# Kernel optimization log

Measured on AMD Instinct MI355X. Metric: run time of the kernel, lower is better.

The kernel has to match this reference:

```python
import jax, jax.numpy as jnp
import numpy as np

N_TYPES = 4
N_DESC = 8
K_MAX = 8
R_C = 5.0
L_MAX = 4
N_ATOMS = 10000
M_NBR = 20


def chebyshev_basis(r, r_c, k_max):
    fc = jnp.where(r < r_c, 0.5 * jnp.cos(jnp.pi * r / r_c) + 0.5, jnp.zeros_like(r))
    x = 2.0 * (r / r_c - 1.0) ** 2 - 1.0
    fn = [jnp.ones_like(x), x]
    for _ in range(2, k_max):
        fn.append(2.0 * x * fn[-1] - fn[-2])
    fn = jnp.stack(fn[:k_max], axis=-1)  # [T, k_max]
    return (fn + 1.0) * (0.5 * fc)[..., None]


def legendre_basis(cos_theta, l_max):
    pl = [jnp.ones_like(cos_theta), cos_theta]
    for l in range(2, l_max):
        pl.append(((2 * l - 1) * cos_theta * pl[-1] - (l - 1) * pl[-2]) / l)
    return jnp.stack(pl[:l_max], axis=-1)  # [T, l_max]


def setup_inputs() -> dict:
    key = jax.random.key(0)
    k1, k2, k3, k4 = jax.random.split(key, 4)
    types = jax.random.randint(k1, (N_ATOMS,), 0, N_TYPES)
    # small box so pair distances mostly fall under the cutoff r_c
    positions = jax.random.uniform(k2, (N_ATOMS, 3), dtype=jnp.float32) * 4.0
    # all neighbor slots valid (no -1 padding) and never the atom itself
    offs = jax.random.randint(k3, (N_ATOMS, M_NBR), 1, N_ATOMS)
    angular_neighbors = (jnp.arange(N_ATOMS)[:, None] + offs) % N_ATOMS
    c_table = jax.random.normal(k4, (N_TYPES, N_TYPES, N_DESC, K_MAX), dtype=jnp.float32)
    return {"types": types, "positions": positions,
            "angular_neighbors": angular_neighbors, "c_table": c_table}


def reference(types, positions, angular_neighbors, c_table):
    N, M = angular_neighbors.shape
    ju, ku = np.triu_indices(M, 1)  # P = M*(M-1)//2 pairs per atom
    P = ju.shape[0]
    j_idx = angular_neighbors[:, ju].reshape(-1)  # [N*P]
    k_idx = angular_neighbors[:, ku].reshape(-1)
    i_idx = jnp.repeat(jnp.arange(N), P)

    pos_i = positions[i_idx]
    rij = positions[j_idx] - pos_i
    rik = positions[k_idx] - pos_i
    r_ij = jnp.linalg.norm(rij, axis=-1)
    r_ik = jnp.linalg.norm(rik, axis=-1)
    cos_theta = jnp.sum(rij * rik, axis=-1) / (r_ij * r_ik + 1e-8)

    type_i = types[i_idx]
    f_ij = chebyshev_basis(r_ij, R_C, K_MAX)  # [T, k]
    f_ik = chebyshev_basis(r_ik, R_C, K_MAX)
    c_ij = c_table[type_i, types[j_idx]]  # [T, n_desc, k]
    c_ik = c_table[type_i, types[k_idx]]
    g_ij = jnp.einsum('tdk,tk->td', c_ij, f_ij)  # [T, n_desc]
    g_ik = jnp.einsum('tdk,tk->td', c_ik, f_ik)

    P_l = legendre_basis(cos_theta, L_MAX)  # [T, l_max]
    ang = (g_ij * g_ik)[:, :, None] * P_l[:, None, :]  # [T, n_desc, l_max]
    q = jax.ops.segment_sum(ang, i_idx, num_segments=N)  # [N, n_desc, l_max]
    return q
```

## Files before the change

kernel.cpp:

```cpp
#include <hip/hip_runtime.h>

#define N_TYPES 4
#define N_DESC  8
#define K_MAX   8
#define L_MAX   4
#define M_NBR   20
#define NCOMP   20
#define ATOMS_PER_BLOCK 4

constexpr float R_C  = 5.0f;
constexpr float SQ2  = 1.41421356237309515f;
constexpr float SQ3  = 1.73205080756887729f;
constexpr float SQ6  = 2.44948974968163702f;

__global__ __launch_bounds__(256) void AngularDescriptor_kernel(
    const int*   __restrict__ types,
    const float* __restrict__ pos,
    const int*   __restrict__ nbr,
    const float* __restrict__ c_table,
    float*       __restrict__ out,
    int N)
{
    __shared__ float sfeat[ATOMS_PER_BLOCK][NCOMP][M_NBR];
    __shared__ float scheb[ATOMS_PER_BLOCK][M_NBR][K_MAX];
    __shared__ float sg   [ATOMS_PER_BLOCK][N_DESC][M_NBR];
    __shared__ int   stj  [ATOMS_PER_BLOCK][M_NBR];

    const int t    = threadIdx.x;
    const int w    = t >> 6;
    const int lane = t & 63;
    const int atom = blockIdx.x * ATOMS_PER_BLOCK + w;

    float px = 0.f, py = 0.f, pz = 0.f;
    int ti = 0;
    if (atom < N) {
        ti = types[atom];
        px = pos[atom * 3 + 0];
        py = pos[atom * 3 + 1];
        pz = pos[atom * 3 + 2];
    }

    if (atom < N && lane < M_NBR) {
        const int j = nbr[atom * M_NBR + lane];
        const float dx = pos[j * 3 + 0] - px;
        const float dy = pos[j * 3 + 1] - py;
        const float dz = pos[j * 3 + 2] - pz;
        const float r2   = dx * dx + dy * dy + dz * dz;
        const float rinv = __builtin_amdgcn_rsqf(r2);
        const float r    = r2 * rinv;

        const float fc  = (r < R_C) ? (0.5f * __builtin_amdgcn_cosf(r * (0.5f / R_C)) + 0.5f)
                                    : 0.0f;
        const float hfc = 0.5f * fc;
        const float u   = r * (1.0f / R_C) - 1.0f;
        const float x   = 2.0f * u * u - 1.0f;
        float ch[K_MAX];
        ch[0] = 2.0f * hfc;
        ch[1] = (x + 1.0f) * hfc;
        float tkm2 = 1.0f, tkm1 = x;
        #pragma unroll
        for (int k = 2; k < K_MAX; ++k) {
            const float tk = 2.0f * x * tkm1 - tkm2;
            ch[k] = (tk + 1.0f) * hfc;
            tkm2 = tkm1; tkm1 = tk;
        }
        ((float4*)&scheb[w][lane][0])[0] = make_float4(ch[0], ch[1], ch[2], ch[3]);
        ((float4*)&scheb[w][lane][0])[1] = make_float4(ch[4], ch[5], ch[6], ch[7]);
        stj[w][lane] = types[j];

        const float ux = dx * rinv, uy = dy * rinv, uz = dz * rinv;
        const float x2 = ux * ux, y2 = uy * uy, z2 = uz * uz;
        float F[NCOMP];
        F[0]  = 1.0f;
        F[1]  = ux;  F[2] = uy;  F[3] = uz;
        F[4]  = x2 - (1.0f / 3.0f);
        F[5]  = y2 - (1.0f / 3.0f);
        F[6]  = z2 - (1.0f / 3.0f);
        F[7]  = SQ2 * ux * uy;
        F[8]  = SQ2 * ux * uz;
        F[9]  = SQ2 * uy * uz;
        F[10] = ux * (x2 - 0.6f);
        F[11] = uy * (y2 - 0.6f);
        F[12] = uz * (z2 - 0.6f);
        F[13] = SQ3 * uy * (x2 - 0.2f);
        F[14] = SQ3 * uz * (x2 - 0.2f);
        F[15] = SQ3 * ux * (y2 - 0.2f);
        F[16] = SQ3 * uz * (y2 - 0.2f);
        F[17] = SQ3 * ux * (z2 - 0.2f);
        F[18] = SQ3 * uy * (z2 - 0.2f);
        F[19] = SQ6 * ux * uy * uz;
        #pragma unroll
        for (int c = 0; c < NCOMP; ++c) sfeat[w][c][lane] = F[c];
    }
    __syncthreads();

    const int d  = lane & 7;
    const int gp = lane >> 3;

    if (atom < N) {
        #pragma unroll
        for (int m = gp; m < M_NBR; m += 8) {
            const int tj = stj[w][m];
            const float* c = c_table + (((ti * N_TYPES + tj) * N_DESC + d) * K_MAX);
            const float4 c0 = ((const float4*)c)[0];
            const float4 c1 = ((const float4*)c)[1];
            const float4 f0 = ((const float4*)&scheb[w][m][0])[0];
            const float4 f1 = ((const float4*)&scheb[w][m][0])[1];
            sg[w][d][m] = c0.x * f0.x + c0.y * f0.y + c0.z * f0.z + c0.w * f0.w
                        + c1.x * f1.x + c1.y * f1.y + c1.z * f1.z + c1.w * f1.w;
        }
    }
    __syncthreads();

    float p0 = 0.f, p1 = 0.f, p2 = 0.f, p3 = 0.f;
    float hG2 = 0.f;
    if (atom < N) {
        float g[M_NBR];
        #pragma unroll
        for (int i = 0; i < 5; ++i) {
            const float4 v = ((const float4*)&sg[w][d][0])[i];
            g[4*i+0] = v.x; g[4*i+1] = v.y; g[4*i+2] = v.z; g[4*i+3] = v.w;
        }
        float G2 = 0.f;
        #pragma unroll
        for (int m = 0; m < M_NBR; ++m) G2 = fmaf(g[m], g[m], G2);
        hG2 = 0.5f * G2;

        #pragma unroll
        for (int s = 0; s < 3; ++s) {
            const int c = gp + 8 * s;
            if (c < NCOMP) {
                float acc = 0.f;
                #pragma unroll
                for (int i = 0; i < 5; ++i) {
                    const float4 v = ((const float4*)&sfeat[w][c][0])[i];
                    acc = fmaf(g[4*i+0], v.x, acc);
                    acc = fmaf(g[4*i+1], v.y, acc);
                    acc = fmaf(g[4*i+2], v.z, acc);
                    acc = fmaf(g[4*i+3], v.w, acc);
                }
                const float v2 = acc * acc;
                if      (c == 0)  p0 += 0.50f * v2;
                else if (c <= 3)  p1 += 0.50f * v2;
                else if (c <= 9)  p2 += 0.75f * v2;
                else              p3 += 1.25f * v2;
            }
        }
    }

    #pragma unroll
    for (int off = 8; off <= 32; off <<= 1) {
        p0 += __shfl_xor(p0, off, 64);
        p1 += __shfl_xor(p1, off, 64);
        p2 += __shfl_xor(p2, off, 64);
        p3 += __shfl_xor(p3, off, 64);
    }

    if (atom < N && lane < 8) {
        ((float4*)out)[atom * N_DESC + d] =
            make_float4(p0 - hG2, p1 - hG2, p2 - hG2, p3 - hG2);
    }
}

extern "C" void kernel_launch(void* const* d_in, const int* in_sizes, int n_in,
                              void* d_out, int out_size, void* d_ws, size_t ws_size,
                              hipStream_t stream) {
    const int*   types   = (const int*)  d_in[0];
    const float* pos     = (const float*)d_in[1];
    const int*   nbr     = (const int*)  d_in[2];
    const float* c_table = (const float*)d_in[3];
    float*       out     = (float*)      d_out;

    const int N = in_sizes[0];
    const int grid = (N + ATOMS_PER_BLOCK - 1) / ATOMS_PER_BLOCK;
    AngularDescriptor_kernel<<<grid, 256, 0, stream>>>(types, pos, nbr, c_table, out, N);
}
```

Measured before the change: 66.08 us.

## Pack 16 atoms per block with flat neighbor work distribution and per-thread accumulation

Replaces the one-wavefront-per-atom mapping, where 44 of 64 lanes sat idle in the neighbor phase, with a flat loop over 16 atoms x 20 neighbors spread across all 256 threads. Each neighbor thread now computes its 8 descriptor projections directly from the Chebyshev basis, which removes one barrier phase and the scheb/stj shared buffers. The final phase gives each (atom, desc) pair to one thread that accumulates all 20 angular components in registers, replacing the shuffle reduction. Shared-memory writes are rotated to reduce bank conflicts. In exchange, only 128 of 256 threads are active in the last phase and register pressure rises.

```diff
diff --git a/kernel.cpp b/kernel.cpp
--- a/kernel.cpp
+++ b/kernel.cpp
@@ -3,17 +3,18 @@
 #define N_TYPES 4
 #define N_DESC  8
 #define K_MAX   8
-#define L_MAX   4
 #define M_NBR   20
 #define NCOMP   20
-#define ATOMS_PER_BLOCK 4
+#define ATOMS   16
+#define BLOCK   256
+#define P1_ITEMS (ATOMS * M_NBR)
 
-constexpr float R_C  = 5.0f;
-constexpr float SQ2  = 1.41421356237309515f;
-constexpr float SQ3  = 1.73205080756887729f;
-constexpr float SQ6  = 2.44948974968163702f;
+constexpr float R_C = 5.0f;
+constexpr float SQ2 = 1.41421356237309515f;
+constexpr float SQ3 = 1.73205080756887729f;
+constexpr float SQ6 = 2.44948974968163702f;
 
-__global__ __launch_bounds__(256) void AngularDescriptor_kernel(
+__global__ __launch_bounds__(BLOCK) void AngularDescriptor_kernel(
     const int*   __restrict__ types,
     const float* __restrict__ pos,
     const int*   __restrict__ nbr,
@@ -21,144 +22,135 @@
     float*       __restrict__ out,
     int N)
 {
-    __shared__ float sfeat[ATOMS_PER_BLOCK][NCOMP][M_NBR];
-    __shared__ float scheb[ATOMS_PER_BLOCK][M_NBR][K_MAX];
-    __shared__ float sg   [ATOMS_PER_BLOCK][N_DESC][M_NBR];
-    __shared__ int   stj  [ATOMS_PER_BLOCK][M_NBR];
+    __shared__ float sF[ATOMS][M_NBR][NCOMP];
+    __shared__ float sg[ATOMS][N_DESC][M_NBR];
 
-    const int t    = threadIdx.x;
-    const int w    = t >> 6;
-    const int lane = t & 63;
-    const int atom = blockIdx.x * ATOMS_PER_BLOCK + w;
+    const int t     = threadIdx.x;
+    const int atom0 = blockIdx.x * ATOMS;
 
-    float px = 0.f, py = 0.f, pz = 0.f;
-    int ti = 0;
-    if (atom < N) {
-        ti = types[atom];
-        px = pos[atom * 3 + 0];
-        py = pos[atom * 3 + 1];
-        pz = pos[atom * 3 + 2];
-    }
+    for (int e = t; e < P1_ITEMS; e += BLOCK) {
+        const int a    = e / M_NBR;
+        const int m    = e - a * M_NBR;
+        const int atom = atom0 + a;
+        if (atom < N) {
+            const int j  = nbr[atom * M_NBR + m];
+            const int ti = types[atom];
+            const int tj = types[j];
+            const float dx = pos[j * 3 + 0] - pos[atom * 3 + 0];
+            const float dy = pos[j * 3 + 1] - pos[atom * 3 + 1];
+            const float dz = pos[j * 3 + 2] - pos[atom * 3 + 2];
+            const float r2   = dx * dx + dy * dy + dz * dz;
+            const float rinv = __builtin_amdgcn_rsqf(r2);
+            const float r    = r2 * rinv;
 
-    if (atom < N && lane < M_NBR) {
-        const int j = nbr[atom * M_NBR + lane];
-        const float dx = pos[j * 3 + 0] - px;
-        const float dy = pos[j * 3 + 1] - py;
-        const float dz = pos[j * 3 + 2] - pz;
-        const float r2   = dx * dx + dy * dy + dz * dz;
-        const float rinv = __builtin_amdgcn_rsqf(r2);
-        const float r    = r2 * rinv;
+            const float fc  = (r < R_C)
+                ? (0.5f * __builtin_amdgcn_cosf(r * (0.5f / R_C)) + 0.5f) : 0.0f;
+            const float hfc = 0.5f * fc;
+            const float u   = r * (1.0f / R_C) - 1.0f;
+            const float x   = 2.0f * u * u - 1.0f;
+            float ch[K_MAX];
+            ch[0] = 2.0f * hfc;
+            ch[1] = (x + 1.0f) * hfc;
+            float tkm2 = 1.0f, tkm1 = x;
+            #pragma unroll
+            for (int k = 2; k < K_MAX; ++k) {
+                const float tk = 2.0f * x * tkm1 - tkm2;
+                ch[k] = (tk + 1.0f) * hfc;
+                tkm2 = tkm1; tkm1 = tk;
+            }
 
-        const float fc  = (r < R_C) ? (0.5f * __builtin_amdgcn_cosf(r * (0.5f / R_C)) + 0.5f)
-                                    : 0.0f;
-        const float hfc = 0.5f * fc;
-        const float u   = r * (1.0f / R_C) - 1.0f;
-        const float x   = 2.0f * u * u - 1.0f;
-        float ch[K_MAX];
-        ch[0] = 2.0f * hfc;
-        ch[1] = (x + 1.0f) * hfc;
-        float tkm2 = 1.0f, tkm1 = x;
-        #pragma unroll
-        for (int k = 2; k < K_MAX; ++k) {
-            const float tk = 2.0f * x * tkm1 - tkm2;
-            ch[k] = (tk + 1.0f) * hfc;
-            tkm2 = tkm1; tkm1 = tk;
-        }
-        ((float4*)&scheb[w][lane][0])[0] = make_float4(ch[0], ch[1], ch[2], ch[3]);
-        ((float4*)&scheb[w][lane][0])[1] = make_float4(ch[4], ch[5], ch[6], ch[7]);
-        stj[w][lane] = types[j];
+            const float* crow = c_table + (ti * N_TYPES + tj) * (N_DESC * K_MAX);
+            float g[N_DESC];
+            #pragma unroll
+            for (int d = 0; d < N_DESC; ++d) {
+                const float4 c0 = ((const float4*)crow)[2 * d + 0];
+                const float4 c1 = ((const float4*)crow)[2 * d + 1];
+                g[d] = c0.x * ch[0] + c0.y * ch[1] + c0.z * ch[2] + c0.w * ch[3]
+                     + c1.x * ch[4] + c1.y * ch[5] + c1.z * ch[6] + c1.w * ch[7];
+            }
+            #pragma unroll
+            for (int dd = 0; dd < N_DESC; ++dd) {
+                const int d = (dd + a) & 7;
+                sg[a][d][m] = g[d];
+            }
 
-        const float ux = dx * rinv, uy = dy * rinv, uz = dz * rinv;
-        const float x2 = ux * ux, y2 = uy * uy, z2 = uz * uz;
-        float F[NCOMP];
-        F[0]  = 1.0f;
-        F[1]  = ux;  F[2] = uy;  F[3] = uz;
-        F[4]  = x2 - (1.0f / 3.0f);
-        F[5]  = y2 - (1.0f / 3.0f);
-        F[6]  = z2 - (1.0f / 3.0f);
-        F[7]  = SQ2 * ux * uy;
-        F[8]  = SQ2 * ux * uz;
-        F[9]  = SQ2 * uy * uz;
-        F[10] = ux * (x2 - 0.6f);
-        F[11] = uy * (y2 - 0.6f);
-        F[12] = uz * (z2 - 0.6f);
-        F[13] = SQ3 * uy * (x2 - 0.2f);
-        F[14] = SQ3 * uz * (x2 - 0.2f);
-        F[15] = SQ3 * ux * (y2 - 0.2f);
-        F[16] = SQ3 * uz * (y2 - 0.2f);
-        F[17] = SQ3 * ux * (z2 - 0.2f);
-        F[18] = SQ3 * uy * (z2 - 0.2f);
-        F[19] = SQ6 * ux * uy * uz;
-        #pragma unroll
-        for (int c = 0; c < NCOMP; ++c) sfeat[w][c][lane] = F[c];
-    }
-    __syncthreads();
-
-    const int d  = lane & 7;
-    const int gp = lane >> 3;
-
-    if (atom < N) {
-        #pragma unroll
-        for (int m = gp; m < M_NBR; m += 8) {
-            const int tj = stj[w][m];
-            const float* c = c_table + (((ti * N_TYPES + tj) * N_DESC + d) * K_MAX);
-            const float4 c0 = ((const float4*)c)[0];
-            const float4 c1 = ((const float4*)c)[1];
-            const float4 f0 = ((const float4*)&scheb[w][m][0])[0];
-            const float4 f1 = ((const float4*)&scheb[w][m][0])[1];
-            sg[w][d][m] = c0.x * f0.x + c0.y * f0.y + c0.z * f0.z + c0.w * f0.w
-                        + c1.x * f1.x + c1.y * f1.y + c1.z * f1.z + c1.w * f1.w;
+            const float ux = dx * rinv, uy = dy * rinv, uz = dz * rinv;
+            const float x2 = ux * ux, y2 = uy * uy, z2 = uz * uz;
+            float F[NCOMP];
+            F[0]  = 1.0f;
+            F[1]  = ux;  F[2] = uy;  F[3] = uz;
+            F[4]  = x2 - (1.0f / 3.0f);
+            F[5]  = y2 - (1.0f / 3.0f);
+            F[6]  = z2 - (1.0f / 3.0f);
+            F[7]  = SQ2 * ux * uy;
+            F[8]  = SQ2 * ux * uz;
+            F[9]  = SQ2 * uy * uz;
+            F[10] = ux * (x2 - 0.6f);
+            F[11] = uy * (y2 - 0.6f);
+            F[12] = uz * (z2 - 0.6f);
+            F[13] = SQ3 * uy * (x2 - 0.2f);
+            F[14] = SQ3 * uz * (x2 - 0.2f);
+            F[15] = SQ3 * ux * (y2 - 0.2f);
+            F[16] = SQ3 * uz * (y2 - 0.2f);
+            F[17] = SQ3 * ux * (z2 - 0.2f);
+            F[18] = SQ3 * uy * (z2 - 0.2f);
+            F[19] = SQ6 * ux * uy * uz;
+            float4* frow = (float4*)&sF[a][m][0];
+            const int mr = m % 5;
+            #pragma unroll
+            for (int ss = 0; ss < 5; ++ss) {
+                int cc = ss + mr; cc = (cc >= 5) ? cc - 5 : cc;
+                frow[cc] = make_float4(F[4*cc+0], F[4*cc+1], F[4*cc+2], F[4*cc+3]);
+            }
         }
     }
     __syncthreads();
 
-    float p0 = 0.f, p1 = 0.f, p2 = 0.f, p3 = 0.f;
-    float hG2 = 0.f;
-    if (atom < N) {
-        float g[M_NBR];
-        #pragma unroll
-        for (int i = 0; i < 5; ++i) {
-            const float4 v = ((const float4*)&sg[w][d][0])[i];
-            g[4*i+0] = v.x; g[4*i+1] = v.y; g[4*i+2] = v.z; g[4*i+3] = v.w;
-        }
-        float G2 = 0.f;
-        #pragma unroll
-        for (int m = 0; m < M_NBR; ++m) G2 = fmaf(g[m], g[m], G2);
-        hG2 = 0.5f * G2;
+    if (t < ATOMS * N_DESC) {
+        const int a    = t >> 3;
+        const int d    = t & 7;
+        const int atom = atom0 + a;
+        if (atom < N) {
+            float g[M_NBR];
+            const float4* gr = (const float4*)&sg[a][d][0];
+            #pragma unroll
+            for (int i = 0; i < 5; ++i) {
+                const float4 v = gr[i];
+                g[4*i+0] = v.x; g[4*i+1] = v.y; g[4*i+2] = v.z; g[4*i+3] = v.w;
+            }
+            float G2 = 0.f;
+            #pragma unroll
+            for (int m = 0; m < M_NBR; ++m) G2 = fmaf(g[m], g[m], G2);
 
-        #pragma unroll
-        for (int s = 0; s < 3; ++s) {
-            const int c = gp + 8 * s;
-            if (c < NCOMP) {
-                float acc = 0.f;
+            float acc[NCOMP];
+            #pragma unroll
+            for (int c = 0; c < NCOMP; ++c) acc[c] = 0.f;
+            #pragma unroll
+            for (int m = 0; m < M_NBR; ++m) {
+                const float4* Fr = (const float4*)&sF[a][m][0];
+                const float gm = g[m];
                 #pragma unroll
                 for (int i = 0; i < 5; ++i) {
-                    const float4 v = ((const float4*)&sfeat[w][c][0])[i];
-                    acc = fmaf(g[4*i+0], v.x, acc);
-                    acc = fmaf(g[4*i+1], v.y, acc);
-                    acc = fmaf(g[4*i+2], v.z, acc);
-                    acc = fmaf(g[4*i+3], v.w, acc);
+                    const float4 f = Fr[i];
+                    acc[4*i+0] = fmaf(gm, f.x, acc[4*i+0]);
+                    acc[4*i+1] = fmaf(gm, f.y, acc[4*i+1]);
+                    acc[4*i+2] = fmaf(gm, f.z, acc[4*i+2]);
+                    acc[4*i+3] = fmaf(gm, f.w, acc[4*i+3]);
                 }
-                const float v2 = acc * acc;
-                if      (c == 0)  p0 += 0.50f * v2;
-                else if (c <= 3)  p1 += 0.50f * v2;
-                else if (c <= 9)  p2 += 0.75f * v2;
-                else              p3 += 1.25f * v2;
             }
+            float p1 = acc[1]*acc[1] + acc[2]*acc[2] + acc[3]*acc[3];
+            float p2 = 0.f, p3 = 0.f;
+            #pragma unroll
+            for (int c = 4; c < 10; ++c)  p2 = fmaf(acc[c], acc[c], p2);
+            #pragma unroll
+            for (int c = 10; c < 20; ++c) p3 = fmaf(acc[c], acc[c], p3);
+            const float hG2 = 0.5f * G2;
+            ((float4*)out)[atom * N_DESC + d] = make_float4(
+                0.5f  * acc[0] * acc[0] - hG2,
+                0.5f  * p1               - hG2,
+                0.75f * p2               - hG2,
+                1.25f * p3               - hG2);
         }
-    }
-
-    #pragma unroll
-    for (int off = 8; off <= 32; off <<= 1) {
-        p0 += __shfl_xor(p0, off, 64);
-        p1 += __shfl_xor(p1, off, 64);
-        p2 += __shfl_xor(p2, off, 64);
-        p3 += __shfl_xor(p3, off, 64);
-    }
-
-    if (atom < N && lane < 8) {
-        ((float4*)out)[atom * N_DESC + d] =
-            make_float4(p0 - hG2, p1 - hG2, p2 - hG2, p3 - hG2);
     }
 }
 
@@ -172,6 +164,6 @@
     float*       out     = (float*)      d_out;
 
     const int N = in_sizes[0];
-    const int grid = (N + ATOMS_PER_BLOCK - 1) / ATOMS_PER_BLOCK;
-    AngularDescriptor_kernel<<<grid, 256, 0, stream>>>(types, pos, nbr, c_table, out, N);
+    const int grid = (N + ATOMS - 1) / ATOMS;
+    AngularDescriptor_kernel<<<grid, BLOCK, 0, stream>>>(types, pos, nbr, c_table, out, N);
 }
```

New measurement: 73.40 us. 11.1% more time.
